# Optimization experiments

Measured on AMD Instinct MI355X. Metric: run time of the kernel, lower is better.

The kernel has to match this reference:

```python
import jax, jax.numpy as jnp
import numpy as np

N_HEADS = 16

def setup_inputs() -> dict:
    key = jax.random.key(0)
    k1, k2 = jax.random.split(key)
    B, N, D = 2, 2048, 1024
    hidden_states = jax.random.normal(k1, (B, N, D), dtype=jnp.float32)
    # init std = initializer_range / sqrt(2 * num_layers * hidden_size)
    std = 0.02 / np.sqrt(2.0 * 24 * D)
    queries_weight = jax.random.normal(k2, (D, D), dtype=jnp.float32) * std
    return {"hidden_states": hidden_states, "queries_weight": queries_weight}

def reference(hidden_states, queries_weight):
    # DenseAttention, causal quadratic variant, multi-head, no relpe.
    B, N, D = hidden_states.shape
    H = N_HEADS
    hd = D // H
    # Q = X @ Wq, split into heads -> [B, H, N, hd]
    q = (hidden_states @ queries_weight).reshape(B, N, H, hd).transpose(0, 2, 1, 3)
    # K provided transposed per head -> [B, H, hd, N]; V -> [B, H, N, hd]
    xh = hidden_states.reshape(B, N, H, hd)
    k = xh.transpose(0, 2, 3, 1)
    v = xh.transpose(0, 2, 1, 3)
    # pre_attn = tril(Q @ K)  (no softmax in DenseAttention)
    pre_attn = jnp.tril(jnp.einsum('bhnd,bhdm->bhnm', q, k))  # [B,H,N,N]
    attn = jnp.einsum('bhnm,bhmd->bhnd', pre_attn, v)          # [B,H,N,hd]
    return attn.transpose(0, 2, 1, 3).reshape(B, N, D)
```

## Files before the change

### kernel.cpp

```cpp
#include <hip/hip_runtime.h>
#include <stdint.h>

#define Bz 2
#define Nseq 2048
#define Dm 1024
#define Hh 16
#define NCHUNK 32
#define BKq 64

typedef _Float16 half_t;
typedef __attribute__((ext_vector_type(8))) _Float16 h8v;
typedef __attribute__((ext_vector_type(4))) _Float16 h4v;
typedef __attribute__((ext_vector_type(4))) float f4v;

#define GLDS(g, l)                                                        \
  __builtin_amdgcn_global_load_lds(                                       \
      (const __attribute__((address_space(1))) void*)(g),                 \
      (__attribute__((address_space(3))) void*)(l), 16, 0, 0)

__global__ __launch_bounds__(256) void prep_fused(const float* __restrict__ X,
                                                  const float* __restrict__ W,
                                                  half_t* __restrict__ Xf,
                                                  half_t* __restrict__ U16,
                                                  half_t* __restrict__ WT) {
  __shared__ double smem_[2304];
  int bx = blockIdx.x;
  int t = threadIdx.x;
  if (bx < 1024) {
    half_t(*xt)[72] = (half_t(*)[72])smem_;
    half_t(*xtT)[72] = (half_t(*)[72])(smem_ + 1152);
    int c = bx & 31, h = (bx >> 5) & 15, b = bx >> 9;
    int r = t >> 2, c16 = (t & 3) * 16;
    {
      const float* src = X + ((size_t)b * Nseq + c * 64 + r) * Dm + h * 64 + c16;
      half_t* dXf = Xf + ((size_t)b * Nseq + c * 64 + r) * Dm + h * 64 + c16;
      h8v v0, v1;
#pragma unroll
      for (int j = 0; j < 8; j++) { v0[j] = (half_t)src[j]; v1[j] = (half_t)src[8 + j]; }
      *(h8v*)&xt[r][c16] = v0;
      *(h8v*)&xt[r][c16 + 8] = v1;
      *(h8v*)&dXf[0] = v0;
      *(h8v*)&dXf[8] = v1;
    }
    __syncthreads();
    {
      int d = r, mg = c16;
      h8v v0, v1;
#pragma unroll
      for (int j = 0; j < 8; j++) { v0[j] = xt[mg + j][d]; v1[j] = xt[mg + 8 + j][d]; }
      *(h8v*)&xtT[d][mg] = v0;
      *(h8v*)&xtT[d][mg + 8] = v1;
    }
    __syncthreads();
    int wave = t >> 6, lane = t & 63;
    int lrow = lane & 15, lk = (lane >> 4) * 8;
    h8v a0 = *(h8v*)&xtT[wave * 16 + lrow][lk];
    h8v a1 = *(h8v*)&xtT[wave * 16 + lrow][32 + lk];
    f4v acc[4] = {};
#pragma unroll
    for (int j = 0; j < 4; j++) {
      acc[j] = __builtin_amdgcn_mfma_f32_16x16x32_f16(a0, *(h8v*)&xtT[j * 16 + lrow][lk], acc[j], 0, 0, 0);
      acc[j] = __builtin_amdgcn_mfma_f32_16x16x32_f16(a1, *(h8v*)&xtT[j * 16 + lrow][32 + lk], acc[j], 0, 0, 0);
    }
    half_t* ub = U16 + (size_t)bx * 4096;
#pragma unroll
    for (int j = 0; j < 4; j++)
#pragma unroll
      for (int v = 0; v < 4; v++)
        ub[(size_t)(wave * 16 + (lane >> 4) * 4 + v) * 64 + j * 16 + (lane & 15)] = (half_t)acc[j][v];
  } else {
    float(*tile)[65] = (float(*)[65])smem_;
    int bw = bx - 1024;
    int tk = bw >> 4, tn = bw & 15;
    int r = t >> 2, c0 = (t & 3) * 16;
    const float* src = W + (size_t)(tk * 64 + r) * Dm + tn * 64 + c0;
#pragma unroll
    for (int j = 0; j < 16; j++) tile[r][c0 + j] = src[j];
    __syncthreads();
    half_t* dst = WT + (size_t)(tn * 64 + r) * Dm + tk * 64 + c0;
    h8v v0, v1;
#pragma unroll
    for (int j = 0; j < 8; j++) {
      v0[j] = (half_t)(tile[c0 + j][r] * 4096.0f);
      v1[j] = (half_t)(tile[c0 + 8 + j][r] * 4096.0f);
    }
    *(h8v*)&dst[0] = v0;
    *(h8v*)&dst[8] = v1;
  }
}

__global__ __launch_bounds__(256) void prefix16(const half_t* __restrict__ U16,
                                                half_t* __restrict__ S16) {
  int g = blockIdx.x * 256 + threadIdx.x;
  int bh = g >> 10, e4 = g & 1023;
  const half_t* u = U16 + (size_t)bh * NCHUNK * 4096 + e4 * 4;
  half_t* s = S16 + (size_t)bh * NCHUNK * 4096 + e4 * 4;
  float r0 = 0, r1 = 0, r2 = 0, r3 = 0;
  for (int c = 0; c < NCHUNK; c++) {
    h4v sv;
    sv[0] = (half_t)r0; sv[1] = (half_t)r1; sv[2] = (half_t)r2; sv[3] = (half_t)r3;
    *(h4v*)(s + (size_t)c * 4096) = sv;
    h4v uv = *(const h4v*)(u + (size_t)c * 4096);
    r0 += (float)uv[0]; r1 += (float)uv[1]; r2 += (float)uv[2]; r3 += (float)uv[3];
  }
}

__global__ __launch_bounds__(256) void qgemm_attn(const half_t* __restrict__ Xf,
                                                  const half_t* __restrict__ WT,
                                                  const half_t* __restrict__ S16,
                                                  float* __restrict__ out) {
  __shared__ __attribute__((aligned(16))) char smem[55296];
  int bid = blockIdx.x;
  int logical = (bid & 7) * 64 + (bid >> 3);
  int bm = logical >> 4;
  int bn = logical & 15;
  int t = threadIdx.x;
  int wave = t >> 6, lane = t & 63;
  int wr = wave >> 1, wc = wave & 1;
  int lrow = lane & 15, g4 = lane >> 4;

  int srowA = wave * 32 + (lane >> 3);
  int srowB = wave * 16 + (lane >> 3);
  int scol = ((lane & 7) ^ (lane >> 3)) * 8;
  const half_t* pA = Xf + (size_t)(bm * 128 + srowA) * Dm + scol;
  const half_t* pB = WT + (size_t)(bn * 64 + srowB) * Dm + scol;

  f4v acc[4][2] = {};
  {
    half_t* dA = (half_t*)(smem) + (wave * 32) * BKq;
    half_t* dB = (half_t*)(smem + 32768) + (wave * 16) * BKq;
#pragma unroll
    for (int q = 0; q < 4; q++) GLDS(pA + (size_t)q * 8 * Dm, dA + q * 8 * BKq);
#pragma unroll
    for (int q = 0; q < 2; q++) GLDS(pB + (size_t)q * 8 * Dm, dB + q * 8 * BKq);
  }
  __syncthreads();
  for (int it = 0; it < 16; ++it) {
    int cur = it & 1;
    if (it < 15) {
      int k1 = (it + 1) * BKq;
      half_t* dA = (half_t*)(smem + (cur ^ 1) * 16384) + (wave * 32) * BKq;
      half_t* dB = (half_t*)(smem + 32768 + (cur ^ 1) * 8192) + (wave * 16) * BKq;
#pragma unroll
      for (int q = 0; q < 4; q++) GLDS(pA + (size_t)q * 8 * Dm + k1, dA + q * 8 * BKq);
#pragma unroll
      for (int q = 0; q < 2; q++) GLDS(pB + (size_t)q * 8 * Dm + k1, dB + q * 8 * BKq);
    }
    const char* cA = smem + cur * 16384;
    const char* cB = smem + 32768 + cur * 8192;
#pragma unroll
    for (int ks2 = 0; ks2 < 2; ks2++) {
      h8v af[4], bf[2];
#pragma unroll
      for (int i = 0; i < 4; i++) {
        int rA = wr * 64 + i * 16 + lrow;
        uint offA = (uint)rA * 128 + (((uint)(ks2 * 64 + g4 * 16)) ^ (uint)((rA & 7) << 4));
        af[i] = *(const h8v*)(cA + offA);
      }
#pragma unroll
      for (int j = 0; j < 2; j++) {
        int rB = wc * 32 + j * 16 + lrow;
        uint offB = (uint)rB * 128 + (((uint)(ks2 * 64 + g4 * 16)) ^ (uint)((rB & 7) << 4));
        bf[j] = *(const h8v*)(cB + offB);
      }
#pragma unroll
      for (int i = 0; i < 4; i++)
#pragma unroll
        for (int j = 0; j < 2; j++)
          acc[i][j] = __builtin_amdgcn_mfma_f32_16x16x32_f16(af[i], bf[j], acc[i][j], 0, 0, 0);
    }
    __syncthreads();
  }

  half_t(*qs0)[72] = (half_t(*)[72])(smem);
  half_t(*qs1)[72] = (half_t(*)[72])(smem + 9216);
  half_t(*ks)[72]  = (half_t(*)[72])(smem + 18432);
  half_t(*vts)[72] = (half_t(*)[72])(smem + 27648);
  half_t(*ss)[72]  = (half_t(*)[72])(smem + 36864);
  half_t(*pt)[72]  = (half_t(*)[72])(smem + 46080);
  {
    half_t(*qsw)[72] = wr ? qs1 : qs0;
#pragma unroll
    for (int i = 0; i < 4; i++)
#pragma unroll
      for (int j = 0; j < 2; j++)
#pragma unroll
        for (int v = 0; v < 4; v++)
          qsw[i * 16 + (lane >> 4) * 4 + v][wc * 32 + j * 16 + (lane & 15)] =
              (half_t)(acc[i][j][v] * 0.0625f);
  }
  int r = t >> 2, c16 = (t & 3) * 16;
  int lk = g4 * 8;
  int h = bn;
  for (int cc = 0; cc < 2; ++cc) {
    if (cc) __syncthreads();
    int gc = bm * 2 + cc;
    int b = gc >> 5, cl = gc & 31;
    {
      size_t rowoff = ((size_t)b * Nseq + cl * 64 + r) * Dm + h * 64 + c16;
      *(h8v*)&ks[r][c16]     = *(const h8v*)(Xf + rowoff);
      *(h8v*)&ks[r][c16 + 8] = *(const h8v*)(Xf + rowoff + 8);
      size_t soff = ((size_t)(b * Hh + h) * NCHUNK + cl) * 4096 + r * 64 + c16;
      *(h8v*)&ss[r][c16]     = *(const h8v*)(S16 + soff);
      *(h8v*)&ss[r][c16 + 8] = *(const h8v*)(S16 + soff + 8);
    }
    __syncthreads();
    half_t(*qsc)[72] = cc ? qs1 : qs0;
    h8v aq0 = *(h8v*)&qsc[wave * 16 + lrow][lk];
    h8v aq1 = *(h8v*)&qsc[wave * 16 + lrow][32 + lk];
    f4v p[4] = {};
#pragma unroll
    for (int j = 0; j < 4; j++) {
      p[j] = __builtin_amdgcn_mfma_f32_16x16x32_f16(aq0, *(h8v*)&ks[j * 16 + lrow][lk], p[j], 0, 0, 0);
      p[j] = __builtin_amdgcn_mfma_f32_16x16x32_f16(aq1, *(h8v*)&ks[j * 16 + lrow][32 + lk], p[j], 0, 0, 0);
    }
    {
      int d = r, mg = c16;
      h8v v0, v1;
#pragma unroll
      for (int jj = 0; jj < 8; jj++) { v0[jj] = ks[mg + jj][d]; v1[jj] = ks[mg + 8 + jj][d]; }
      *(h8v*)&vts[d][mg] = v0;
      *(h8v*)&vts[d][mg + 8] = v1;
    }
    int orow = wave * 16 + (lane >> 4) * 4;
#pragma unroll
    for (int j = 0; j < 4; j++)
#pragma unroll
      for (int v = 0; v < 4; v++) {
        int rr = orow + v, mm = j * 16 + (lane & 15);
        pt[rr][mm] = (half_t)((mm <= rr) ? p[j][v] : 0.f);
      }
    __syncthreads();
    h8v ap0 = *(h8v*)&pt[wave * 16 + lrow][lk];
    h8v ap1 = *(h8v*)&pt[wave * 16 + lrow][32 + lk];
    f4v o[4] = {};
#pragma unroll
    for (int j = 0; j < 4; j++) {
      o[j] = __builtin_amdgcn_mfma_f32_16x16x32_f16(ap0, *(h8v*)&vts[j * 16 + lrow][lk], o[j], 0, 0, 0);
      o[j] = __builtin_amdgcn_mfma_f32_16x16x32_f16(ap1, *(h8v*)&vts[j * 16 + lrow][32 + lk], o[j], 0, 0, 0);
      o[j] = __builtin_amdgcn_mfma_f32_16x16x32_f16(aq0, *(h8v*)&ss[j * 16 + lrow][lk], o[j], 0, 0, 0);
      o[j] = __builtin_amdgcn_mfma_f32_16x16x32_f16(aq1, *(h8v*)&ss[j * 16 + lrow][32 + lk], o[j], 0, 0, 0);
    }
    float* dst = out + ((size_t)b * Nseq + cl * 64) * Dm + h * 64;
#pragma unroll
    for (int j = 0; j < 4; j++)
#pragma unroll
      for (int v = 0; v < 4; v++)
        dst[(size_t)(orow + v) * Dm + j * 16 + (lane & 15)] = o[j][v] * 0.00390625f;
  }
}

extern "C" void kernel_launch(void* const* d_in, const int* in_sizes, int n_in,
                              void* d_out, int out_size, void* d_ws, size_t ws_size,
                              hipStream_t stream) {
  const float* X = (const float*)d_in[0];
  const float* W = (const float*)d_in[1];
  float* out = (float*)d_out;

  half_t* U16 = (half_t*)d_ws;
  half_t* Xf = U16 + 4194304;
  half_t* S16 = Xf + 4194304;
  half_t* WT = S16 + 4194304;

  prep_fused<<<1280, 256, 0, stream>>>(X, W, Xf, U16, WT);
  prefix16<<<128, 256, 0, stream>>>(U16, S16);
  qgemm_attn<<<512, 256, 0, stream>>>(Xf, WT, S16, out);
}
```

Baseline: 96.49 us.

## Split GEMM K-dimension across wave pairs with LDS reduction of partial Q

Changes the wave decomposition of the Q-projection GEMM. Each wave pair now covers the full 64-column N tile and splits the 64-wide K slice between its two waves, instead of splitting N. This halves the A-fragment LDS reads per MFMA and doubles the accumulator tile per wave. It costs a float scratch reduction through shared memory plus an extra barrier, and the LDS layout of the attention buffers is reshuffled to avoid clobbering the Q tiles.

```diff
diff --git a/kernel.cpp b/kernel.cpp
--- a/kernel.cpp
+++ b/kernel.cpp
@@ -116,7 +116,7 @@
   int bn = logical & 15;
   int t = threadIdx.x;
   int wave = t >> 6, lane = t & 63;
-  int wr = wave >> 1, wc = wave & 1;
+  int wr = wave >> 1, wk = wave & 1;
   int lrow = lane & 15, g4 = lane >> 4;
 
   int srowA = wave * 32 + (lane >> 3);
@@ -125,7 +125,7 @@
   const half_t* pA = Xf + (size_t)(bm * 128 + srowA) * Dm + scol;
   const half_t* pB = WT + (size_t)(bn * 64 + srowB) * Dm + scol;
 
-  f4v acc[4][2] = {};
+  f4v acc[4][4] = {};
   {
     half_t* dA = (half_t*)(smem) + (wave * 32) * BKq;
     half_t* dB = (half_t*)(smem + 32768) + (wave * 16) * BKq;
@@ -148,47 +148,61 @@
     }
     const char* cA = smem + cur * 16384;
     const char* cB = smem + 32768 + cur * 8192;
-#pragma unroll
-    for (int ks2 = 0; ks2 < 2; ks2++) {
-      h8v af[4], bf[2];
-#pragma unroll
-      for (int i = 0; i < 4; i++) {
-        int rA = wr * 64 + i * 16 + lrow;
-        uint offA = (uint)rA * 128 + (((uint)(ks2 * 64 + g4 * 16)) ^ (uint)((rA & 7) << 4));
-        af[i] = *(const h8v*)(cA + offA);
-      }
-#pragma unroll
-      for (int j = 0; j < 2; j++) {
-        int rB = wc * 32 + j * 16 + lrow;
-        uint offB = (uint)rB * 128 + (((uint)(ks2 * 64 + g4 * 16)) ^ (uint)((rB & 7) << 4));
-        bf[j] = *(const h8v*)(cB + offB);
-      }
+    uint koff = (uint)(wk * 64 + g4 * 16);
+    h8v af[4], bf[4];
+#pragma unroll
+    for (int i = 0; i < 4; i++) {
+      int rA = wr * 64 + i * 16 + lrow;
+      af[i] = *(const h8v*)(cA + (uint)rA * 128 + (koff ^ (uint)((rA & 7) << 4)));
+    }
+#pragma unroll
+    for (int j = 0; j < 4; j++) {
+      int rB = j * 16 + lrow;
+      bf[j] = *(const h8v*)(cB + (uint)rB * 128 + (koff ^ (uint)((rB & 7) << 4)));
+    }
+#pragma unroll
+    for (int i = 0; i < 4; i++)
+#pragma unroll
+      for (int j = 0; j < 4; j++)
+        acc[i][j] = __builtin_amdgcn_mfma_f32_16x16x32_f16(af[i], bf[j], acc[i][j], 0, 0, 0);
+    __syncthreads();
+  }
+
+  half_t(*qs0)[72] = (half_t(*)[72])(smem + 36864);
+  half_t(*qs1)[72] = (half_t(*)[72])(smem + 46080);
+  {
+    float* scratch = (float*)smem;
+    if (wk) {
 #pragma unroll
       for (int i = 0; i < 4; i++)
 #pragma unroll
-        for (int j = 0; j < 2; j++)
-          acc[i][j] = __builtin_amdgcn_mfma_f32_16x16x32_f16(af[i], bf[j], acc[i][j], 0, 0, 0);
-    }
-    __syncthreads();
-  }
-
-  half_t(*qs0)[72] = (half_t(*)[72])(smem);
-  half_t(*qs1)[72] = (half_t(*)[72])(smem + 9216);
-  half_t(*ks)[72]  = (half_t(*)[72])(smem + 18432);
-  half_t(*vts)[72] = (half_t(*)[72])(smem + 27648);
-  half_t(*ss)[72]  = (half_t(*)[72])(smem + 36864);
-  half_t(*pt)[72]  = (half_t(*)[72])(smem + 46080);
-  {
-    half_t(*qsw)[72] = wr ? qs1 : qs0;
-#pragma unroll
-    for (int i = 0; i < 4; i++)
-#pragma unroll
-      for (int j = 0; j < 2; j++)
-#pragma unroll
-        for (int v = 0; v < 4; v++)
-          qsw[i * 16 + (lane >> 4) * 4 + v][wc * 32 + j * 16 + (lane & 15)] =
-              (half_t)(acc[i][j][v] * 0.0625f);
-  }
+        for (int j = 0; j < 4; j++)
+#pragma unroll
+          for (int v = 0; v < 4; v++)
+            scratch[(wr * 64 + i * 16 + (lane >> 4) * 4 + v) * 66 + j * 16 + (lane & 15)] =
+                acc[i][j][v];
+    }
+    __syncthreads();
+    if (!wk) {
+      half_t(*qsw)[72] = wr ? qs1 : qs0;
+#pragma unroll
+      for (int i = 0; i < 4; i++)
+#pragma unroll
+        for (int j = 0; j < 4; j++)
+#pragma unroll
+          for (int v = 0; v < 4; v++) {
+            int rr = i * 16 + (lane >> 4) * 4 + v, ccol = j * 16 + (lane & 15);
+            float s = acc[i][j][v] + scratch[(wr * 64 + rr) * 66 + ccol];
+            qsw[rr][ccol] = (half_t)(s * 0.0625f);
+          }
+    }
+  }
+  __syncthreads();
+
+  half_t(*ks)[72]  = (half_t(*)[72])(smem);
+  half_t(*vts)[72] = (half_t(*)[72])(smem + 9216);
+  half_t(*ss)[72]  = (half_t(*)[72])(smem + 18432);
+  half_t(*pt)[72]  = (half_t(*)[72])(smem + 27648);
   int r = t >> 2, c16 = (t & 3) * 16;
   int lk = g4 * 8;
   int h = bn;
```

After: 97.89 us. No clear change (+1.5%).

## Fuse chunk prefix-sum into attention kernel, drop separate prefix16 launch

Applied to the files above, without the earlier changes.

Removes the prefix16 kernel and the S16 workspace. Each qgemm_attn block now sums the per-chunk K^T V state matrices of all earlier chunks itself, in float registers, before it processes its own chunks. This drops one kernel launch and the S16 write and read round-trip. In exchange, blocks for later chunks do up to 31 redundant global reads each, so the total prefix work is repeated across many blocks.

```diff
diff --git a/kernel.cpp b/kernel.cpp
--- a/kernel.cpp
+++ b/kernel.cpp
@@ -89,25 +89,9 @@
   }
 }
 
-__global__ __launch_bounds__(256) void prefix16(const half_t* __restrict__ U16,
-                                                half_t* __restrict__ S16) {
-  int g = blockIdx.x * 256 + threadIdx.x;
-  int bh = g >> 10, e4 = g & 1023;
-  const half_t* u = U16 + (size_t)bh * NCHUNK * 4096 + e4 * 4;
-  half_t* s = S16 + (size_t)bh * NCHUNK * 4096 + e4 * 4;
-  float r0 = 0, r1 = 0, r2 = 0, r3 = 0;
-  for (int c = 0; c < NCHUNK; c++) {
-    h4v sv;
-    sv[0] = (half_t)r0; sv[1] = (half_t)r1; sv[2] = (half_t)r2; sv[3] = (half_t)r3;
-    *(h4v*)(s + (size_t)c * 4096) = sv;
-    h4v uv = *(const h4v*)(u + (size_t)c * 4096);
-    r0 += (float)uv[0]; r1 += (float)uv[1]; r2 += (float)uv[2]; r3 += (float)uv[3];
-  }
-}
-
 __global__ __launch_bounds__(256) void qgemm_attn(const half_t* __restrict__ Xf,
                                                   const half_t* __restrict__ WT,
-                                                  const half_t* __restrict__ S16,
+                                                  const half_t* __restrict__ U16,
                                                   float* __restrict__ out) {
   __shared__ __attribute__((aligned(16))) char smem[55296];
   int bid = blockIdx.x;
@@ -172,12 +156,12 @@
     __syncthreads();
   }
 
-  half_t(*qs0)[72] = (half_t(*)[72])(smem);
-  half_t(*qs1)[72] = (half_t(*)[72])(smem + 9216);
-  half_t(*ks)[72]  = (half_t(*)[72])(smem + 18432);
-  half_t(*vts)[72] = (half_t(*)[72])(smem + 27648);
-  half_t(*ss)[72]  = (half_t(*)[72])(smem + 36864);
-  half_t(*pt)[72]  = (half_t(*)[72])(smem + 46080);
+  half_t(*ks)[72]  = (half_t(*)[72])(smem);
+  half_t(*vts)[72] = (half_t(*)[72])(smem + 9216);
+  half_t(*ss)[72]  = (half_t(*)[72])(smem + 18432);
+  half_t(*pt)[72]  = (half_t(*)[72])(smem + 27648);
+  half_t(*qs0)[72] = (half_t(*)[72])(smem + 36864);
+  half_t(*qs1)[72] = (half_t(*)[72])(smem + 46080);
   {
     half_t(*qsw)[72] = wr ? qs1 : qs0;
 #pragma unroll
@@ -189,20 +173,41 @@
           qsw[i * 16 + (lane >> 4) * 4 + v][wc * 32 + j * 16 + (lane & 15)] =
               (half_t)(acc[i][j][v] * 0.0625f);
   }
+
   int r = t >> 2, c16 = (t & 3) * 16;
   int lk = g4 * 8;
   int h = bn;
+  int gc0 = bm * 2;
+  int b = gc0 >> 5, cl0 = gc0 & 31;
+
+  float sacc[16] = {};
+  const half_t* ubase =
+      U16 + ((size_t)(b * Hh + h) * NCHUNK) * 4096 + r * 64 + c16;
+  for (int cp = 0; cp < cl0; cp++) {
+    h8v u0 = *(const h8v*)(ubase + (size_t)cp * 4096);
+    h8v u1 = *(const h8v*)(ubase + (size_t)cp * 4096 + 8);
+#pragma unroll
+    for (int j = 0; j < 8; j++) { sacc[j] += (float)u0[j]; sacc[8 + j] += (float)u1[j]; }
+  }
+
   for (int cc = 0; cc < 2; ++cc) {
-    if (cc) __syncthreads();
-    int gc = bm * 2 + cc;
-    int b = gc >> 5, cl = gc & 31;
-    {
+    if (cc) {
+      __syncthreads();
+      h8v u0 = *(const h8v*)(ubase + (size_t)cl0 * 4096);
+      h8v u1 = *(const h8v*)(ubase + (size_t)cl0 * 4096 + 8);
+#pragma unroll
+      for (int j = 0; j < 8; j++) { sacc[j] += (float)u0[j]; sacc[8 + j] += (float)u1[j]; }
+    }
+    int cl = cl0 + cc;
+    {
+      h8v s0, s1;
+#pragma unroll
+      for (int j = 0; j < 8; j++) { s0[j] = (half_t)sacc[j]; s1[j] = (half_t)sacc[8 + j]; }
+      *(h8v*)&ss[r][c16] = s0;
+      *(h8v*)&ss[r][c16 + 8] = s1;
       size_t rowoff = ((size_t)b * Nseq + cl * 64 + r) * Dm + h * 64 + c16;
       *(h8v*)&ks[r][c16]     = *(const h8v*)(Xf + rowoff);
       *(h8v*)&ks[r][c16 + 8] = *(const h8v*)(Xf + rowoff + 8);
-      size_t soff = ((size_t)(b * Hh + h) * NCHUNK + cl) * 4096 + r * 64 + c16;
-      *(h8v*)&ss[r][c16]     = *(const h8v*)(S16 + soff);
-      *(h8v*)&ss[r][c16 + 8] = *(const h8v*)(S16 + soff + 8);
     }
     __syncthreads();
     half_t(*qsc)[72] = cc ? qs1 : qs0;
@@ -259,10 +264,8 @@
 
   half_t* U16 = (half_t*)d_ws;
   half_t* Xf = U16 + 4194304;
-  half_t* S16 = Xf + 4194304;
-  half_t* WT = S16 + 4194304;
+  half_t* WT = Xf + 4194304;
 
   prep_fused<<<1280, 256, 0, stream>>>(X, W, Xf, U16, WT);
-  prefix16<<<128, 256, 0, stream>>>(U16, S16);
-  qgemm_attn<<<512, 256, 0, stream>>>(Xf, WT, S16, out);
+  qgemm_attn<<<512, 256, 0, stream>>>(Xf, WT, U16, out);
 }
```

Result: slower. 98.79 us (+2.4%).

## Load fp32 X directly in Q GEMM, convert in-kernel, drop fp16 X copy

Applied to the files above, without the earlier changes.

The prep kernel no longer writes an fp16 copy of X. The Q GEMM instead loads fp32 X through registers and converts it with packed round-toward-zero conversions before storing it to swizzled LDS. When the K-loop reaches the tile that matches this block's head, the attention K tile is captured from LDS. This removes a full fp16 write and re-read of X, but it replaces async global-to-LDS loads with register-staged loads that read twice the bytes. It also raises LDS use to about 66KB, which may lower occupancy, and switches rounding to truncation.

```diff
diff --git a/kernel.cpp b/kernel.cpp
--- a/kernel.cpp
+++ b/kernel.cpp
@@ -9,18 +9,29 @@
 #define BKq 64
 
 typedef _Float16 half_t;
+typedef __attribute__((ext_vector_type(2))) __fp16 fp16x2;
 typedef __attribute__((ext_vector_type(8))) _Float16 h8v;
 typedef __attribute__((ext_vector_type(4))) _Float16 h4v;
 typedef __attribute__((ext_vector_type(4))) float f4v;
+
+struct fp16x8 { fp16x2 p[4]; };
 
 #define GLDS(g, l)                                                        \
   __builtin_amdgcn_global_load_lds(                                       \
       (const __attribute__((address_space(1))) void*)(g),                 \
       (__attribute__((address_space(3))) void*)(l), 16, 0, 0)
 
+__device__ __forceinline__ h8v cvt8(const float4& a, const float4& b) {
+  fp16x8 r;
+  r.p[0] = __builtin_amdgcn_cvt_pkrtz(a.x, a.y);
+  r.p[1] = __builtin_amdgcn_cvt_pkrtz(a.z, a.w);
+  r.p[2] = __builtin_amdgcn_cvt_pkrtz(b.x, b.y);
+  r.p[3] = __builtin_amdgcn_cvt_pkrtz(b.z, b.w);
+  return __builtin_bit_cast(h8v, r);
+}
+
 __global__ __launch_bounds__(256) void prep_fused(const float* __restrict__ X,
                                                   const float* __restrict__ W,
-                                                  half_t* __restrict__ Xf,
                                                   half_t* __restrict__ U16,
                                                   half_t* __restrict__ WT) {
   __shared__ double smem_[2304];
@@ -33,14 +44,11 @@
     int r = t >> 2, c16 = (t & 3) * 16;
     {
       const float* src = X + ((size_t)b * Nseq + c * 64 + r) * Dm + h * 64 + c16;
-      half_t* dXf = Xf + ((size_t)b * Nseq + c * 64 + r) * Dm + h * 64 + c16;
       h8v v0, v1;
 #pragma unroll
       for (int j = 0; j < 8; j++) { v0[j] = (half_t)src[j]; v1[j] = (half_t)src[8 + j]; }
       *(h8v*)&xt[r][c16] = v0;
       *(h8v*)&xt[r][c16 + 8] = v1;
-      *(h8v*)&dXf[0] = v0;
-      *(h8v*)&dXf[8] = v1;
     }
     __syncthreads();
     {
@@ -105,11 +113,11 @@
   }
 }
 
-__global__ __launch_bounds__(256) void qgemm_attn(const half_t* __restrict__ Xf,
+__global__ __launch_bounds__(256) void qgemm_attn(const float* __restrict__ X,
                                                   const half_t* __restrict__ WT,
                                                   const half_t* __restrict__ S16,
                                                   float* __restrict__ out) {
-  __shared__ __attribute__((aligned(16))) char smem[55296];
+  __shared__ __attribute__((aligned(16))) char smem[67584];
   int bid = blockIdx.x;
   int logical = (bid & 7) * 64 + (bid >> 3);
   int bm = logical >> 4;
@@ -119,30 +127,46 @@
   int wr = wave >> 1, wc = wave & 1;
   int lrow = lane & 15, g4 = lane >> 4;
 
-  int srowA = wave * 32 + (lane >> 3);
+  half_t(*ks0)[72] = (half_t(*)[72])(smem + 49152);
+  half_t(*ks1)[72] = (half_t(*)[72])(smem + 58368);
+
+  const float* pAbase =
+      X + (size_t)(bm * 128 + wave * 32 + (lane >> 3)) * Dm + (lane & 7) * 8;
+  int rl0 = wave * 32 + (lane >> 3);
+  uint swzA = ((uint)(lane & 7) * 16) ^ ((uint)((lane >> 3) & 7) << 4);
   int srowB = wave * 16 + (lane >> 3);
   int scol = ((lane & 7) ^ (lane >> 3)) * 8;
-  const half_t* pA = Xf + (size_t)(bm * 128 + srowA) * Dm + scol;
   const half_t* pB = WT + (size_t)(bn * 64 + srowB) * Dm + scol;
 
   f4v acc[4][2] = {};
   {
-    half_t* dA = (half_t*)(smem) + (wave * 32) * BKq;
+    float4 ra[4][2];
+#pragma unroll
+    for (int q = 0; q < 4; q++) {
+      ra[q][0] = *(const float4*)(pAbase + (size_t)q * 8 * Dm);
+      ra[q][1] = *(const float4*)(pAbase + (size_t)q * 8 * Dm + 4);
+    }
     half_t* dB = (half_t*)(smem + 32768) + (wave * 16) * BKq;
 #pragma unroll
-    for (int q = 0; q < 4; q++) GLDS(pA + (size_t)q * 8 * Dm, dA + q * 8 * BKq);
-#pragma unroll
     for (int q = 0; q < 2; q++) GLDS(pB + (size_t)q * 8 * Dm, dB + q * 8 * BKq);
+#pragma unroll
+    for (int q = 0; q < 4; q++) {
+      h8v hv = cvt8(ra[q][0], ra[q][1]);
+      *(h8v*)(smem + (uint)(rl0 + q * 8) * 128 + swzA) = hv;
+    }
   }
   __syncthreads();
   for (int it = 0; it < 16; ++it) {
     int cur = it & 1;
+    float4 ra[4][2];
     if (it < 15) {
       int k1 = (it + 1) * BKq;
-      half_t* dA = (half_t*)(smem + (cur ^ 1) * 16384) + (wave * 32) * BKq;
+#pragma unroll
+      for (int q = 0; q < 4; q++) {
+        ra[q][0] = *(const float4*)(pAbase + (size_t)q * 8 * Dm + k1);
+        ra[q][1] = *(const float4*)(pAbase + (size_t)q * 8 * Dm + k1 + 4);
+      }
       half_t* dB = (half_t*)(smem + 32768 + (cur ^ 1) * 8192) + (wave * 16) * BKq;
-#pragma unroll
-      for (int q = 0; q < 4; q++) GLDS(pA + (size_t)q * 8 * Dm + k1, dA + q * 8 * BKq);
 #pragma unroll
       for (int q = 0; q < 2; q++) GLDS(pB + (size_t)q * 8 * Dm + k1, dB + q * 8 * BKq);
     }
@@ -169,15 +193,36 @@
         for (int j = 0; j < 2; j++)
           acc[i][j] = __builtin_amdgcn_mfma_f32_16x16x32_f16(af[i], bf[j], acc[i][j], 0, 0, 0);
     }
-    __syncthreads();
-  }
-
-  half_t(*qs0)[72] = (half_t(*)[72])(smem);
-  half_t(*qs1)[72] = (half_t(*)[72])(smem + 9216);
-  half_t(*ks)[72]  = (half_t(*)[72])(smem + 18432);
-  half_t(*vts)[72] = (half_t(*)[72])(smem + 27648);
-  half_t(*ss)[72]  = (half_t(*)[72])(smem + 36864);
-  half_t(*pt)[72]  = (half_t(*)[72])(smem + 46080);
+    if (it == bn) {
+      int r = t >> 2;
+      int cb0 = (t & 3) * 32;
+#pragma unroll
+      for (int half = 0; half < 2; half++) {
+        int rr = r + half * 64;
+        uint sw = (uint)((rr & 7) << 4);
+        h8v v0 = *(const h8v*)(cA + (uint)rr * 128 + ((uint)cb0 ^ sw));
+        h8v v1 = *(const h8v*)(cA + (uint)rr * 128 + ((uint)(cb0 + 16) ^ sw));
+        half_t(*kdst)[72] = half ? ks1 : ks0;
+        *(h8v*)&kdst[r][(t & 3) * 16] = v0;
+        *(h8v*)&kdst[r][(t & 3) * 16 + 8] = v1;
+      }
+    }
+    if (it < 15) {
+      char* dA = smem + (cur ^ 1) * 16384;
+#pragma unroll
+      for (int q = 0; q < 4; q++) {
+        h8v hv = cvt8(ra[q][0], ra[q][1]);
+        *(h8v*)(dA + (uint)(rl0 + q * 8) * 128 + swzA) = hv;
+      }
+    }
+    __syncthreads();
+  }
+
+  half_t(*vts)[72] = (half_t(*)[72])(smem);
+  half_t(*ss)[72]  = (half_t(*)[72])(smem + 9216);
+  half_t(*pt)[72]  = (half_t(*)[72])(smem + 18432);
+  half_t(*qs0)[72] = (half_t(*)[72])(smem + 27648);
+  half_t(*qs1)[72] = (half_t(*)[72])(smem + 36864);
   {
     half_t(*qsw)[72] = wr ? qs1 : qs0;
 #pragma unroll
@@ -189,20 +234,27 @@
           qsw[i * 16 + (lane >> 4) * 4 + v][wc * 32 + j * 16 + (lane & 15)] =
               (half_t)(acc[i][j][v] * 0.0625f);
   }
+
   int r = t >> 2, c16 = (t & 3) * 16;
   int lk = g4 * 8;
   int h = bn;
   for (int cc = 0; cc < 2; ++cc) {
-    if (cc) __syncthreads();
     int gc = bm * 2 + cc;
     int b = gc >> 5, cl = gc & 31;
+    if (cc) __syncthreads();
     {
-      size_t rowoff = ((size_t)b * Nseq + cl * 64 + r) * Dm + h * 64 + c16;
-      *(h8v*)&ks[r][c16]     = *(const h8v*)(Xf + rowoff);
-      *(h8v*)&ks[r][c16 + 8] = *(const h8v*)(Xf + rowoff + 8);
       size_t soff = ((size_t)(b * Hh + h) * NCHUNK + cl) * 4096 + r * 64 + c16;
       *(h8v*)&ss[r][c16]     = *(const h8v*)(S16 + soff);
       *(h8v*)&ss[r][c16 + 8] = *(const h8v*)(S16 + soff + 8);
+    }
+    half_t(*ksc)[72] = cc ? ks1 : ks0;
+    {
+      int d = r, mg = c16;
+      h8v v0, v1;
+#pragma unroll
+      for (int jj = 0; jj < 8; jj++) { v0[jj] = ksc[mg + jj][d]; v1[jj] = ksc[mg + 8 + jj][d]; }
+      *(h8v*)&vts[d][mg] = v0;
+      *(h8v*)&vts[d][mg + 8] = v1;
     }
     __syncthreads();
     half_t(*qsc)[72] = cc ? qs1 : qs0;
@@ -211,16 +263,8 @@
     f4v p[4] = {};
 #pragma unroll
     for (int j = 0; j < 4; j++) {
-      p[j] = __builtin_amdgcn_mfma_f32_16x16x32_f16(aq0, *(h8v*)&ks[j * 16 + lrow][lk], p[j], 0, 0, 0);
-      p[j] = __builtin_amdgcn_mfma_f32_16x16x32_f16(aq1, *(h8v*)&ks[j * 16 + lrow][32 + lk], p[j], 0, 0, 0);
-    }
-    {
-      int d = r, mg = c16;
-      h8v v0, v1;
-#pragma unroll
-      for (int jj = 0; jj < 8; jj++) { v0[jj] = ks[mg + jj][d]; v1[jj] = ks[mg + 8 + jj][d]; }
-      *(h8v*)&vts[d][mg] = v0;
-      *(h8v*)&vts[d][mg + 8] = v1;
+      p[j] = __builtin_amdgcn_mfma_f32_16x16x32_f16(aq0, *(h8v*)&ksc[j * 16 + lrow][lk], p[j], 0, 0, 0);
+      p[j] = __builtin_amdgcn_mfma_f32_16x16x32_f16(aq1, *(h8v*)&ksc[j * 16 + lrow][32 + lk], p[j], 0, 0, 0);
     }
     int orow = wave * 16 + (lane >> 4) * 4;
 #pragma unroll
@@ -258,11 +302,10 @@
   float* out = (float*)d_out;
 
   half_t* U16 = (half_t*)d_ws;
-  half_t* Xf = U16 + 4194304;
-  half_t* S16 = Xf + 4194304;
+  half_t* S16 = U16 + 4194304;
   half_t* WT = S16 + 4194304;
 
-  prep_fused<<<1280, 256, 0, stream>>>(X, W, Xf, U16, WT);
+  prep_fused<<<1280, 256, 0, stream>>>(X, W, U16, WT);
   prefix16<<<128, 256, 0, stream>>>(U16, S16);
-  qgemm_attn<<<512, 256, 0, stream>>>(Xf, WT, S16, out);
-}
+  qgemm_attn<<<512, 256, 0, stream>>>(X, WT, S16, out);
+}
```

After: 103.7 us. +7.4%, slower.
